# Kernel optimization log

Hardware: AMD Instinct MI355X
Metric: run time of the kernel (lower is better)

Reference implementation:

```python
import jax, jax.numpy as jnp
import numpy as np

B, L, D, H = 2, 2048, 512, 8
Dh = D // H


def setup_inputs() -> dict:
    key = jax.random.key(0)
    ks = jax.random.split(key, 12)
    def lin(i):
        W = jax.random.normal(ks[i], (D, D), dtype=jnp.float32) * (1.0 / np.sqrt(D))
        b = jax.random.normal(ks[i + 1], (D,), dtype=jnp.float32) * 0.02
        return W, b
    Wq, bq = lin(0)
    Wk, bk = lin(2)
    Wv, bv = lin(4)
    Wo, bo = lin(6)
    wave_real = jax.random.normal(ks[8], (B, L, D), dtype=jnp.float32)
    wave_imag = jax.random.normal(ks[9], (B, L, D), dtype=jnp.float32)
    return {"wave_real": wave_real, "wave_imag": wave_imag,
            "Wq": Wq, "bq": bq, "Wk": Wk, "bk": bk,
            "Wv": Wv, "bv": bv, "Wo": Wo, "bo": bo}


def _heads(x):
    # (B,L,D) -> (B,H,L,Dh)
    return x.reshape(B, L, H, Dh).transpose(0, 2, 1, 3)


def reference(wave_real, wave_imag, Wq, bq, Wk, bk, Wv, bv, Wo, bo):
    Qr = _heads(wave_real @ Wq.T + bq)
    Qi = _heads(wave_imag @ Wq.T + bq)
    Kr = _heads(wave_real @ Wk.T + bk)
    Ki = _heads(wave_imag @ Wk.T + bk)
    Vr = _heads(wave_real @ Wv.T + bv)
    Vi = _heads(wave_imag @ Wv.T + bv)

    inner_real = jnp.einsum('bhid,bhjd->bhij', Qr, Kr) + jnp.einsum('bhid,bhjd->bhij', Qi, Ki)
    inner_imag = jnp.einsum('bhid,bhjd->bhij', Qr, Ki) - jnp.einsum('bhid,bhjd->bhij', Qi, Kr)

    scores = (inner_real ** 2 + inner_imag ** 2) / np.sqrt(Dh).astype(np.float32)
    attention = jax.nn.softmax(scores, axis=-1)

    phase = jnp.arctan2(inner_imag, inner_real)
    ac = attention * jnp.cos(phase)  # (B,H,L,L)
    as_ = attention * jnp.sin(phase)

    # sum_j att_ij*(Vr_j*cos_ij - Vi_j*sin_ij) -- fused contraction, same math as
    # the original's materialized (B,H,L,L,Dh) rotate-then-sum.
    out_real = jnp.einsum('bhij,bhjd->bhid', ac, Vr) - jnp.einsum('bhij,bhjd->bhid', as_, Vi)
    out_imag = jnp.einsum('bhij,bhjd->bhid', as_, Vr) + jnp.einsum('bhij,bhjd->bhid', ac, Vi)

    out_real = out_real.transpose(0, 2, 1, 3).reshape(B, L, D)
    out_imag = out_imag.transpose(0, 2, 1, 3).reshape(B, L, D)
    return (out_real @ Wo.T + bo, out_imag @ Wo.T + bo, attention)
```

## Files before the change

kernel.cpp:

```cpp
#include <hip/hip_runtime.h>

typedef unsigned short u16;
typedef unsigned int   u32;
typedef __attribute__((ext_vector_type(4)))  u16   us4;
typedef __attribute__((ext_vector_type(8)))  u16   us8;
typedef __attribute__((ext_vector_type(8)))  short s8v;
typedef __attribute__((ext_vector_type(16))) float f32x16;

#define L_   2048
#define D_   512
#define H_   8
#define PE_  2097152ull

#define MATE    2097152ull
#define BHE     131072u
#define VT_OFF  33554432ull
#define ORH_OFF 41943040ull
#define ORL_OFF 46137344ull
#define OIH_OFF 50331648ull
#define OIL_OFF 54525952ull
#define LV_OFF  58720256ull

#define XRH_O 16777216ull
#define XRL_O 20971520ull
#define XIH_O 25165824ull
#define XIL_O 29360128ull

#define MFMA32(a,b,c) __builtin_amdgcn_mfma_f32_32x32x16_bf16(a,b,c,0,0,0)
#define ROWOF(r,hi) (((r)&3) + 8*((r)>>2) + 4*(hi))

__device__ __forceinline__ u16 f2bf(float x){
    u32 u = __float_as_uint(x);
    u += 0x7FFFu + ((u>>16)&1u);
    return (u16)(u>>16);
}
__device__ __forceinline__ float bf2f(u16 h){ return __uint_as_float(((u32)h)<<16); }

__device__ __forceinline__ void glds16(const void* gsrc, void* ldst)
{
    __builtin_amdgcn_global_load_lds(
        (const __attribute__((address_space(1))) u32*)(unsigned long long)gsrc,
        (__attribute__((address_space(3))) u32*)(u32)(unsigned long long)ldst,
        16, 0, 0);
}
__device__ __forceinline__ void glds_mat(unsigned char* Lp, u32 matOff,
                                         const u16* g, int rowBase, int lane)
{
    const char* gb = (const char*)(g + (size_t)rowBase * 64);
    #pragma unroll
    for (int s = 0; s < 8; ++s)
        glds16(gb + s*1024 + lane*16, Lp + matOff + s*1024);
}
__device__ __forceinline__ void glds_vt(unsigned char* Lp, u32 matOff,
                                        const u16* g, int j0, int lane, int s0)
{
    #pragma unroll
    for (int s = 0; s < 4; ++s) {
        int seg = s0 + s;
        int dh  = seg*8 + (lane >> 3);
        const char* gp = (const char*)g + (size_t)dh*4096 + (size_t)j0*2 + (lane & 7)*16;
        glds16(gp, Lp + matOff + seg*1024u);
    }
}

__global__ __launch_bounds__(256)
void split_prep_kernel(const float* __restrict__ wr, const float* __restrict__ wi,
                       unsigned char* __restrict__ outb)
{
    const int z = blockIdx.y;
    const float* src = z ? wi : wr;
    u16* hg = (u16*)(outb + (z ? XIH_O : XRH_O));
    u16* lg = (u16*)(outb + (z ? XIL_O : XRL_O));
    const size_t idx4 = ((size_t)blockIdx.x * 256 + threadIdx.x) * 4;
    float4 v = *(const float4*)&src[idx4];
    float vv[4] = { v.x, v.y, v.z, v.w };
    us4 h, l;
    #pragma unroll
    for (int c = 0; c < 4; ++c) {
        u16 hb = f2bf(vv[c]);
        h[c] = hb;
        l[c] = f2bf(vv[c] - bf2f(hb));
    }
    *(us4*)&hg[idx4] = h;
    *(us4*)&lg[idx4] = l;
}

__device__ __forceinline__ s8v ldfrag(const unsigned char* Lp, u32 matOff, u32 row, u32 colb)
{
    return *(const s8v*)(Lp + matOff + row*128u + (colb ^ ((row&7u)<<4)));
}

__global__ __launch_bounds__(256, 2)
void proj_mfma_kernel(const unsigned char* __restrict__ scr,
                      const float* __restrict__ Wq, const float* __restrict__ Wk,
                      const float* __restrict__ Wv,
                      const float* __restrict__ bq, const float* __restrict__ bk,
                      const float* __restrict__ bv,
                      u16* __restrict__ qk, u16* __restrict__ vt)
{
    const int z = blockIdx.z;
    const u16* Ah_g = (const u16*)(scr + ((z & 1) ? XIH_O : XRH_O));
    const u16* Al_g = (const u16*)(scr + ((z & 1) ? XIL_O : XRL_O));
    const int wsel = z >> 1;
    const float* Wf; const float* bias;
    if (wsel == 0)      { Wf = Wq; bias = bq; }
    else if (wsel == 1) { Wf = Wk; bias = bk; }
    else                { Wf = Wv; bias = bv; }
    const bool four = (wsel < 2);

    const int m0 = blockIdx.x * 128;
    const int n0 = blockIdx.y * 64;

    __shared__ __align__(16) unsigned char L[49152];
    enum : u32 { AH=0, AL=16384, BH=32768, BL=40960 };

    const int tid  = threadIdx.x;
    const int lane = tid & 63;
    const int wid  = tid >> 6;
    const int wr   = wid >> 1, wc = wid & 1;
    const int l31  = lane & 31;
    const int hi   = lane >> 5;
    const u32 rowA0 = (u32)(wr*64 + l31);
    const u32 rowB  = (u32)(wc*32 + l31);

    f32x16 c0, c1;
    #pragma unroll
    for (int r = 0; r < 16; ++r) { c0[r] = 0.f; c1[r] = 0.f; }

    const int ch = tid & 7, r0 = tid >> 3;

    for (int k0 = 0; k0 < 512; k0 += 64) {
        __syncthreads();
        #pragma unroll
        for (int rr = 0; rr < 4; ++rr) {
            u32 row = (u32)(rr*32 + r0);
            u32 dst = row*128u + (((u32)ch<<4) ^ ((row&7u)<<4));
            us8 vh = *(const us8*)(Ah_g + (size_t)(m0 + row)*512 + k0 + ch*8);
            *(us8*)(L + AH + dst) = vh;
            if (four) {
                us8 vl = *(const us8*)(Al_g + (size_t)(m0 + row)*512 + k0 + ch*8);
                *(us8*)(L + AL + dst) = vl;
            }
        }
        #pragma unroll
        for (int rr = 0; rr < 2; ++rr) {
            u32 row = (u32)(rr*32 + r0);
            const float* src = Wf + (size_t)(n0 + row)*512 + k0 + ch*8;
            float4 v0 = *(const float4*)src;
            float4 v1 = *(const float4*)(src + 4);
            float vv[8] = { v0.x,v0.y,v0.z,v0.w, v1.x,v1.y,v1.z,v1.w };
            us8 hv, lv;
            #pragma unroll
            for (int j = 0; j < 8; ++j) {
                u16 hb = f2bf(vv[j]);
                hv[j] = hb;
                lv[j] = f2bf(vv[j] - bf2f(hb));
            }
            u32 dst = row*128u + (((u32)ch<<4) ^ ((row&7u)<<4));
            *(us8*)(L + BH + dst) = hv;
            if (four) *(us8*)(L + BL + dst) = lv;
        }
        __syncthreads();

        #pragma unroll
        for (int ks = 0; ks < 4; ++ks) {
            u32 colb = (u32)(ks*32 + hi*16);
            s8v a0h = ldfrag(L, AH, rowA0,      colb);
            s8v a1h = ldfrag(L, AH, rowA0 + 32, colb);
            s8v bh_ = ldfrag(L, BH, rowB,       colb);
            c0 = MFMA32(a0h, bh_, c0);
            c1 = MFMA32(a1h, bh_, c1);
            if (four) {
                s8v a0l = ldfrag(L, AL, rowA0,      colb);
                s8v a1l = ldfrag(L, AL, rowA0 + 32, colb);
                s8v bl_ = ldfrag(L, BL, rowB,       colb);
                c0 = MFMA32(a0h, bl_, c0); c0 = MFMA32(a0l, bh_, c0); c0 = MFMA32(a0l, bl_, c0);
                c1 = MFMA32(a1h, bl_, c1); c1 = MFMA32(a1l, bh_, c1); c1 = MFMA32(a1l, bl_, c1);
            }
        }
    }

    const int n  = n0 + wc*32 + l31;
    const float bvv = bias[n];
    const int h  = n >> 6, dh = n & 63;

    if (z < 4) {
        u16* hg = qk + (size_t)(2*z)   * MATE;
        u16* lg = qk + (size_t)(2*z+1) * MATE;
        #pragma unroll
        for (int f = 0; f < 2; ++f) {
            const f32x16& c = f ? c1 : c0;
            #pragma unroll
            for (int r = 0; r < 16; ++r) {
                int m  = m0 + wr*64 + 32*f + ROWOF(r, hi);
                int b_ = m >> 11, i = m & 2047;
                size_t idx = (size_t)(b_*8 + h)*BHE + (size_t)i*64 + (dh ^ ((i&7)<<3));
                float v = c[r] + bvv;
                u16 hb = f2bf(v);
                hg[idx] = hb;
                lg[idx] = f2bf(v - bf2f(hb));
            }
        }
    } else {
        u16* vg = vt + (size_t)(z & 1) * MATE;
        #pragma unroll
        for (int f = 0; f < 2; ++f) {
            const f32x16& c = f ? c1 : c0;
            #pragma unroll
            for (int g = 0; g < 4; ++g) {
                int mb = m0 + wr*64 + 32*f + 8*g + 4*hi;
                int b_ = mb >> 11, ib = mb & 2047;
                us4 pv;
                #pragma unroll
                for (int j = 0; j < 4; ++j) pv[j] = f2bf(c[4*g + j] + bvv);
                int ibs = ib ^ ((dh & 7) << 3);
                *(us4*)&vg[(size_t)(b_*8 + h)*BHE + (size_t)dh*2048 + ibs] = pv;
            }
        }
    }
}

__global__ __launch_bounds__(256, 2)
void attn_mfma_kernel(const u16* __restrict__ qk,
                      const u16* __restrict__ vt,
                      float* __restrict__ attnbuf,
                      u16* __restrict__ orh, u16* __restrict__ orl,
                      u16* __restrict__ oih, u16* __restrict__ oil,
                      float* __restrict__ l_out)
{
    const int bh = blockIdx.x;
    const int i0 = blockIdx.y * 64;
    const int tid  = threadIdx.x;
    const int lane = tid & 63;
    const int wid  = tid >> 6;
    const int wr   = wid >> 1, wc = wid & 1;
    const int l31  = lane & 31;
    const int hi   = lane >> 5;
    const u32 rowA = wr*32 + l31;
    const u32 rowB = wc*32 + l31;

    __shared__ __align__(16) unsigned char L[49152];
    enum : u32 { QRH=0, QIH=8192,
                 KRH=16384, KRL=24576, KIH=32768, KIL=40960,
                 VRo=16384, VIo=24576,
                 PAC=32768, PAS=40960 };
    float* sc = (float*)(L + PAC);

    const u16* qrh = qk + 0*MATE + (size_t)bh*BHE;
    const u16* qrl = qk + 1*MATE + (size_t)bh*BHE;
    const u16* qih = qk + 2*MATE + (size_t)bh*BHE;
    const u16* qil = qk + 3*MATE + (size_t)bh*BHE;
    const u16* krh = qk + 4*MATE + (size_t)bh*BHE;
    const u16* krl = qk + 5*MATE + (size_t)bh*BHE;
    const u16* kih = qk + 6*MATE + (size_t)bh*BHE;
    const u16* kil = qk + 7*MATE + (size_t)bh*BHE;
    const u16* vtr = vt + 0*MATE + (size_t)bh*BHE;
    const u16* vti = vt + 1*MATE + (size_t)bh*BHE;

    {
        const u16* qsrc = (wid == 0) ? qrh : (wid == 1) ? qih : (wid == 2) ? qrl : qil;
        const u32  qdst = (wid == 0) ? QRH : (wid == 1) ? QIH : (wid == 2) ? KRH : KRL;
        glds_mat(L, qdst, qsrc, i0, lane);
    }
    __syncthreads();
    s8v qfl[2][4];
    #pragma unroll
    for (int ks = 0; ks < 4; ++ks) {
        u32 colb = (u32)(ks*32 + hi*16);
        qfl[0][ks] = ldfrag(L, KRH, rowA, colb);
        qfl[1][ks] = ldfrag(L, KRL, rowA, colb);
    }

    float mxv[16];
    #pragma unroll
    for (int r = 0; r < 16; ++r) mxv[r] = 0.f;

    const u16* s1src = (wid & 1) ? kih : krh;
    const u32  s1off = 16384u + (u32)wid * 8192u;

    for (int jp = 0; jp < 16; ++jp) {
        __syncthreads();
        glds_mat(L, s1off, s1src, (2*jp + (wid >> 1))*64, lane);
        __syncthreads();
        __builtin_amdgcn_s_setprio(1);
        #pragma unroll
        for (int half = 0; half < 2; ++half) {
            const u32 kR = half ? KIH : KRH;
            const u32 kI = half ? KIL : KRL;
            f32x16 ir, ip, in_;
            #pragma unroll
            for (int r = 0; r < 16; ++r) { ir[r]=0.f; ip[r]=0.f; in_[r]=0.f; }
            #pragma unroll
            for (int ks = 0; ks < 4; ++ks) {
                u32 colb = ks*32 + hi*16;
                s8v aR = ldfrag(L, QRH, rowA, colb);
                s8v aI = ldfrag(L, QIH, rowA, colb);
                s8v bR = ldfrag(L, kR,  rowB, colb);
                s8v bI = ldfrag(L, kI,  rowB, colb);
                ir  = MFMA32(aR, bR, ir);
                ir  = MFMA32(aI, bI, ir);
                ip  = MFMA32(aR, bI, ip);
                in_ = MFMA32(aI, bR, in_);
            }
            #pragma unroll
            for (int r = 0; r < 16; ++r) {
                float xr = ir[r], xi = ip[r] - in_[r];
                float q = xr*xr + xi*xi;
                mxv[r] = fmaxf(mxv[r], q * 0.125f);
            }
        }
        __builtin_amdgcn_s_setprio(0);
    }
    #pragma unroll
    for (int m = 1; m < 32; m <<= 1)
        #pragma unroll
        for (int r = 0; r < 16; ++r) mxv[r] = fmaxf(mxv[r], __shfl_xor(mxv[r], m));

    __syncthreads();
    #pragma unroll
    for (int r = 0; r < 16; ++r)
        if (l31 == r) sc[wc*64 + wr*32 + ROWOF(r,hi)] = mxv[r];
    __syncthreads();
    float mfin[16];
    #pragma unroll
    for (int r = 0; r < 16; ++r) {
        u32 row = wr*32 + ROWOF(r,hi);
        mfin[r] = fmaxf(sc[row], sc[64 + row]);
    }

    f32x16 ore, oim;
    float lp[16];
    #pragma unroll
    for (int r = 0; r < 16; ++r) { ore[r]=0.f; oim[r]=0.f; lp[r]=0.f; }

    const u16* s2src = (wid == 0) ? krh : (wid == 1) ? krl : (wid == 2) ? kih : kil;
    const u32  s2off = 16384u + (u32)wid * 8192u;
    const u16* vsrc  = (wid < 2) ? vtr : vti;
    const u32  voff  = (wid < 2) ? VRo : VIo;
    const int  vseg  = (wid & 1) * 4;

    u16* ebase = (u16*)(attnbuf + (size_t)bh*4194304ull + (size_t)i0*2048);

    for (int jt = 0; jt < 32; ++jt) {
        const int j0 = jt * 64;
        __syncthreads();
        glds_mat(L, s2off, s2src, j0, lane);
        __syncthreads();

        f32x16 ir, ip, in_;
        #pragma unroll
        for (int r = 0; r < 16; ++r) { ir[r]=0.f; ip[r]=0.f; in_[r]=0.f; }
        __builtin_amdgcn_s_setprio(1);
        #pragma unroll
        for (int ks = 0; ks < 4; ++ks) {
            u32 colb = ks*32 + hi*16;
            s8v aRH = ldfrag(L, QRH, rowA, colb);
            s8v aIH = ldfrag(L, QIH, rowA, colb);
            s8v aRL = qfl[0][ks];
            s8v aIL = qfl[1][ks];
            s8v bRH = ldfrag(L, KRH, rowB, colb);
            s8v bRL = ldfrag(L, KRL, rowB, colb);
            s8v bIH = ldfrag(L, KIH, rowB, colb);
            s8v bIL = ldfrag(L, KIL, rowB, colb);
            ir = MFMA32(aRH, bRH, ir); ir = MFMA32(aRH, bRL, ir); ir = MFMA32(aRL, bRH, ir);
            ir = MFMA32(aIH, bIH, ir); ir = MFMA32(aIH, bIL, ir); ir = MFMA32(aIL, bIH, ir);
            ip  = MFMA32(aRH, bIH, ip);  ip  = MFMA32(aRH, bIL, ip);  ip  = MFMA32(aRL, bIH, ip);
            in_ = MFMA32(aIH, bRH, in_); in_ = MFMA32(aIH, bRL, in_); in_ = MFMA32(aIL, bRH, in_);
        }
        __builtin_amdgcn_s_setprio(0);
        __syncthreads();

        glds_vt(L, voff, vsrc, j0, lane, vseg);

        #pragma unroll
        for (int r = 0; r < 16; ++r) {
            float xr = ir[r], xi = ip[r] - in_[r];
            float q  = fmaf(xr, xr, xi*xi);
            float e  = __expf(fmaf(q, 0.125f, -mfin[r]));
            lp[r] += e;
            float iv = rsqrtf(q);
            float t  = e * iv;
            float pc = (q > 0.f) ? xr*t : e;
            float ps = (q > 0.f) ? xi*t : 0.0f;
            u32 rowloc = wr*32 + ROWOF(r,hi);
            ebase[(size_t)rowloc*4096 + j0 + wc*32 + l31] = f2bf(e);
            u32 colb2 = (wc*32 + l31)*2;
            *(u16*)(L + PAC + rowloc*128u + (colb2 ^ ((rowloc&7u)<<4))) = f2bf(pc);
            *(u16*)(L + PAS + rowloc*128u + (colb2 ^ ((rowloc&7u)<<4))) = f2bf(ps);
        }
        __syncthreads();

        __builtin_amdgcn_s_setprio(1);
        #pragma unroll
        for (int ks = 0; ks < 4; ++ks) {
            u32 colb = ks*32 + hi*16;
            s8v aC = ldfrag(L, PAC, rowA, colb);
            s8v aS = ldfrag(L, PAS, rowA, colb);
            s8v vR = ldfrag(L, VRo, rowB, colb);
            s8v vI = ldfrag(L, VIo, rowB, colb);
            s8v vN = vI ^ (short)0x8000;
            ore = MFMA32(aC, vR, ore); ore = MFMA32(aS, vN, ore);
            oim = MFMA32(aS, vR, oim); oim = MFMA32(aC, vI, oim);
        }
        __builtin_amdgcn_s_setprio(0);
    }

    #pragma unroll
    for (int m = 1; m < 32; m <<= 1)
        #pragma unroll
        for (int r = 0; r < 16; ++r) lp[r] += __shfl_xor(lp[r], m);

    __syncthreads();
    #pragma unroll
    for (int r = 0; r < 16; ++r)
        if (l31 == r) sc[wc*64 + wr*32 + ROWOF(r,hi)] = lp[r];
    __syncthreads();

    const int b_ = bh >> 3, h = bh & 7;
    const size_t cb = (size_t)h*64 + wc*32 + l31;
    #pragma unroll
    for (int r = 0; r < 16; ++r) {
        u32 row = wr*32 + ROWOF(r,hi);
        float ls = sc[row] + sc[64 + row];
        if (wc == 0 && l31 == 0) l_out[(size_t)bh*2048 + i0 + row] = ls;
        float inv = 1.0f / ls;
        size_t idx = ((size_t)b_*2048 + i0 + row)*512 + cb;
        float vr = ore[r] * inv;
        float vi = oim[r] * inv;
        u16 hr = f2bf(vr); orh[idx] = hr; orl[idx] = f2bf(vr - bf2f(hr));
        u16 hw = f2bf(vi); oih[idx] = hw; oil[idx] = f2bf(vi - bf2f(hw));
    }
}

__global__ __launch_bounds__(256)
void expand_attn_kernel(float* __restrict__ attnbuf, const float* __restrict__ l)
{
    const int row = blockIdx.x;
    const float inv = 1.f / l[row];
    float* rowf = attnbuf + (size_t)row * 2048;
    const us8 ev = *(const us8*)((const u16*)rowf + threadIdx.x * 8);
    __syncthreads();
    float4 o0, o1;
    o0.x = bf2f(ev[0])*inv; o0.y = bf2f(ev[1])*inv;
    o0.z = bf2f(ev[2])*inv; o0.w = bf2f(ev[3])*inv;
    o1.x = bf2f(ev[4])*inv; o1.y = bf2f(ev[5])*inv;
    o1.z = bf2f(ev[6])*inv; o1.w = bf2f(ev[7])*inv;
    float* dst = rowf + threadIdx.x * 8;
    *(float4*)dst       = o0;
    *(float4*)(dst + 4) = o1;
}

__global__ __launch_bounds__(256, 2)
void oproj_mfma_kernel(const unsigned char* __restrict__ wsb,
                       const float* __restrict__ Wo, const float* __restrict__ bo,
                       float* __restrict__ out)
{
    const int z = blockIdx.z;
    const u16* Ah_g = (const u16*)(wsb + (z ? OIH_OFF : ORH_OFF));
    const u16* Al_g = (const u16*)(wsb + (z ? OIL_OFF : ORL_OFF));
    float* outp = out + (size_t)z * PE_;

    const int m0 = blockIdx.x * 128;
    const int n0 = blockIdx.y * 64;

    __shared__ __align__(16) unsigned char L[49152];
    enum : u32 { AH=0, AL=16384, BH=32768, BL=40960 };

    const int tid  = threadIdx.x;
    const int lane = tid & 63;
    const int wid  = tid >> 6;
    const int wr   = wid >> 1, wc = wid & 1;
    const int l31  = lane & 31;
    const int hi   = lane >> 5;
    const u32 rowA0 = (u32)(wr*64 + l31);
    const u32 rowB  = (u32)(wc*32 + l31);

    f32x16 c0, c1;
    #pragma unroll
    for (int r = 0; r < 16; ++r) { c0[r] = 0.f; c1[r] = 0.f; }

    const int ch = tid & 7, r0 = tid >> 3;

    for (int k0 = 0; k0 < 512; k0 += 64) {
        __syncthreads();
        #pragma unroll
        for (int rr = 0; rr < 4; ++rr) {
            u32 row = (u32)(rr*32 + r0);
            u32 dst = row*128u + (((u32)ch<<4) ^ ((row&7u)<<4));
            us8 vh = *(const us8*)(Ah_g + (size_t)(m0 + row)*512 + k0 + ch*8);
            us8 vl = *(const us8*)(Al_g + (size_t)(m0 + row)*512 + k0 + ch*8);
            *(us8*)(L + AH + dst) = vh;
            *(us8*)(L + AL + dst) = vl;
        }
        #pragma unroll
        for (int rr = 0; rr < 2; ++rr) {
            u32 row = (u32)(rr*32 + r0);
            const float* src = Wo + (size_t)(n0 + row)*512 + k0 + ch*8;
            float4 v0 = *(const float4*)src;
            float4 v1 = *(const float4*)(src + 4);
            float vv[8] = { v0.x,v0.y,v0.z,v0.w, v1.x,v1.y,v1.z,v1.w };
            us8 hv, lv;
            #pragma unroll
            for (int j = 0; j < 8; ++j) {
                u16 hb = f2bf(vv[j]);
                hv[j] = hb;
                lv[j] = f2bf(vv[j] - bf2f(hb));
            }
            u32 dst = row*128u + (((u32)ch<<4) ^ ((row&7u)<<4));
            *(us8*)(L + BH + dst) = hv;
            *(us8*)(L + BL + dst) = lv;
        }
        __syncthreads();

        #pragma unroll
        for (int ks = 0; ks < 4; ++ks) {
            u32 colb = (u32)(ks*32 + hi*16);
            s8v a0h = ldfrag(L, AH, rowA0,      colb);
            s8v a1h = ldfrag(L, AH, rowA0 + 32, colb);
            s8v a0l = ldfrag(L, AL, rowA0,      colb);
            s8v a1l = ldfrag(L, AL, rowA0 + 32, colb);
            s8v bh_ = ldfrag(L, BH, rowB,       colb);
            s8v bl_ = ldfrag(L, BL, rowB,       colb);
            c0 = MFMA32(a0h, bh_, c0); c0 = MFMA32(a0h, bl_, c0); c0 = MFMA32(a0l, bh_, c0);
            c1 = MFMA32(a1h, bh_, c1); c1 = MFMA32(a1h, bl_, c1); c1 = MFMA32(a1l, bh_, c1);
        }
    }

    const int n = n0 + wc*32 + l31;
    const float bvv = bo[n];
    #pragma unroll
    for (int f = 0; f < 2; ++f) {
        const f32x16& c = f ? c1 : c0;
        #pragma unroll
        for (int r = 0; r < 16; ++r) {
            int m = m0 + wr*64 + 32*f + ROWOF(r, hi);
            outp[(size_t)m*512 + n] = c[r] + bvv;
        }
    }
}

extern "C" void kernel_launch(void* const* d_in, const int* in_sizes, int n_in,
                              void* d_out, int out_size, void* d_ws, size_t ws_size,
                              hipStream_t stream)
{
    const float* wave_real = (const float*)d_in[0];
    const float* wave_imag = (const float*)d_in[1];
    const float* Wq = (const float*)d_in[2]; const float* bq = (const float*)d_in[3];
    const float* Wk = (const float*)d_in[4]; const float* bk = (const float*)d_in[5];
    const float* Wv = (const float*)d_in[6]; const float* bv = (const float*)d_in[7];
    const float* Wo = (const float*)d_in[8]; const float* bo = (const float*)d_in[9];
    float* out = (float*)d_out;
    unsigned char* outb = (unsigned char*)d_out;
    unsigned char* wsb  = (unsigned char*)d_ws;

    float* attnbuf = out + 2*PE_;

    split_prep_kernel<<<dim3(2048, 2), dim3(256), 0, stream>>>(wave_real, wave_imag, outb);

    proj_mfma_kernel<<<dim3(32, 8, 6), dim3(256), 0, stream>>>(
        outb, Wq, Wk, Wv, bq, bk, bv,
        (u16*)wsb, (u16*)(wsb + VT_OFF));

    attn_mfma_kernel<<<dim3(16, 32), dim3(256), 0, stream>>>(
        (const u16*)wsb, (const u16*)(wsb + VT_OFF), attnbuf,
        (u16*)(wsb + ORH_OFF), (u16*)(wsb + ORL_OFF),
        (u16*)(wsb + OIH_OFF), (u16*)(wsb + OIL_OFF),
        (float*)(wsb + LV_OFF));

    expand_attn_kernel<<<dim3(32768), dim3(256), 0, stream>>>(
        attnbuf, (const float*)(wsb + LV_OFF));

    oproj_mfma_kernel<<<dim3(32, 8, 2), dim3(256), 0, stream>>>(
        wsb, Wo, bo, out);
}
```

Baseline: 336.2 us.

## Process two key tiles per barrier round in attention passes

Grows LDS from 48KB to 80KB so that each sync round loads and processes 128 keys (two 64-key tiles) instead of 64, in both the max pass (four tiles per round instead of two) and the main softmax/PV pass. This halves the number of __syncthreads barriers and global-to-LDS load rounds per block and gives more independent MFMA work between barriers. The cost is higher LDS use and register pressure from holding two score tiles at once, which may reduce occupancy.

```diff
diff --git a/kernel.cpp b/kernel.cpp
--- a/kernel.cpp
+++ b/kernel.cpp
@@ -51,12 +51,11 @@
     for (int s = 0; s < 8; ++s)
         glds16(gb + s*1024 + lane*16, Lp + matOff + s*1024);
 }
-__device__ __forceinline__ void glds_vt(unsigned char* Lp, u32 matOff,
-                                        const u16* g, int j0, int lane, int s0)
-{
-    #pragma unroll
-    for (int s = 0; s < 4; ++s) {
-        int seg = s0 + s;
+__device__ __forceinline__ void glds_vt_full(unsigned char* Lp, u32 matOff,
+                                             const u16* g, int j0, int lane)
+{
+    #pragma unroll
+    for (int seg = 0; seg < 8; ++seg) {
         int dh  = seg*8 + (lane >> 3);
         const char* gp = (const char*)g + (size_t)dh*4096 + (size_t)j0*2 + (lane & 7)*16;
         glds16(gp, Lp + matOff + seg*1024u);
@@ -239,12 +238,9 @@
     const u32 rowA = wr*32 + l31;
     const u32 rowB = wc*32 + l31;
 
-    __shared__ __align__(16) unsigned char L[49152];
-    enum : u32 { QRH=0, QIH=8192,
-                 KRH=16384, KRL=24576, KIH=32768, KIL=40960,
-                 VRo=16384, VIo=24576,
-                 PAC=32768, PAS=40960 };
-    float* sc = (float*)(L + PAC);
+    __shared__ __align__(16) unsigned char L[81920];
+    enum : u32 { QRH=0, QIH=8192, KB=16384 };
+    float* sc = (float*)(L + KB);
 
     const u16* qrh = qk + 0*MATE + (size_t)bh*BHE;
     const u16* qrl = qk + 1*MATE + (size_t)bh*BHE;
@@ -259,7 +255,7 @@
 
     {
         const u16* qsrc = (wid == 0) ? qrh : (wid == 1) ? qih : (wid == 2) ? qrl : qil;
-        const u32  qdst = (wid == 0) ? QRH : (wid == 1) ? QIH : (wid == 2) ? KRH : KRL;
+        const u32  qdst = (wid == 0) ? QRH : (wid == 1) ? QIH : (wid == 2) ? (KB) : (KB + 8192);
         glds_mat(L, qdst, qsrc, i0, lane);
     }
     __syncthreads();
@@ -267,26 +263,24 @@
     #pragma unroll
     for (int ks = 0; ks < 4; ++ks) {
         u32 colb = (u32)(ks*32 + hi*16);
-        qfl[0][ks] = ldfrag(L, KRH, rowA, colb);
-        qfl[1][ks] = ldfrag(L, KRL, rowA, colb);
+        qfl[0][ks] = ldfrag(L, KB,        rowA, colb);
+        qfl[1][ks] = ldfrag(L, KB + 8192, rowA, colb);
     }
 
     float mxv[16];
     #pragma unroll
     for (int r = 0; r < 16; ++r) mxv[r] = 0.f;
 
-    const u16* s1src = (wid & 1) ? kih : krh;
-    const u32  s1off = 16384u + (u32)wid * 8192u;
-
-    for (int jp = 0; jp < 16; ++jp) {
-        __syncthreads();
-        glds_mat(L, s1off, s1src, (2*jp + (wid >> 1))*64, lane);
+    for (int gp = 0; gp < 8; ++gp) {
+        __syncthreads();
+        glds_mat(L, KB + (u32)(2*wid)*8192u,   krh, (4*gp + wid)*64, lane);
+        glds_mat(L, KB + (u32)(2*wid+1)*8192u, kih, (4*gp + wid)*64, lane);
         __syncthreads();
         __builtin_amdgcn_s_setprio(1);
         #pragma unroll
-        for (int half = 0; half < 2; ++half) {
-            const u32 kR = half ? KIH : KRH;
-            const u32 kI = half ? KIL : KRL;
+        for (int t = 0; t < 4; ++t) {
+            const u32 kR = KB + (u32)(2*t)*8192u;
+            const u32 kI = kR + 8192u;
             f32x16 ir, ip, in_;
             #pragma unroll
             for (int r = 0; r < 16; ++r) { ir[r]=0.f; ip[r]=0.f; in_[r]=0.f; }
@@ -334,47 +328,73 @@
     for (int r = 0; r < 16; ++r) { ore[r]=0.f; oim[r]=0.f; lp[r]=0.f; }
 
     const u16* s2src = (wid == 0) ? krh : (wid == 1) ? krl : (wid == 2) ? kih : kil;
-    const u32  s2off = 16384u + (u32)wid * 8192u;
-    const u16* vsrc  = (wid < 2) ? vtr : vti;
-    const u32  voff  = (wid < 2) ? VRo : VIo;
-    const int  vseg  = (wid & 1) * 4;
+    const u16* vsrc2 = (wid & 1) ? vti : vtr;
 
     u16* ebase = (u16*)(attnbuf + (size_t)bh*4194304ull + (size_t)i0*2048);
 
-    for (int jt = 0; jt < 32; ++jt) {
-        const int j0 = jt * 64;
-        __syncthreads();
-        glds_mat(L, s2off, s2src, j0, lane);
-        __syncthreads();
-
-        f32x16 ir, ip, in_;
-        #pragma unroll
-        for (int r = 0; r < 16; ++r) { ir[r]=0.f; ip[r]=0.f; in_[r]=0.f; }
+    for (int pt = 0; pt < 16; ++pt) {
+        const int j0a = pt*128, j0b = j0a + 64;
+        __syncthreads();
+        glds_mat(L, KB + (u32)wid*8192u,          s2src, j0a, lane);
+        glds_mat(L, KB + 32768u + (u32)wid*8192u, s2src, j0b, lane);
+        __syncthreads();
+
+        f32x16 xra, xia, xrb, xib;
         __builtin_amdgcn_s_setprio(1);
-        #pragma unroll
-        for (int ks = 0; ks < 4; ++ks) {
-            u32 colb = ks*32 + hi*16;
-            s8v aRH = ldfrag(L, QRH, rowA, colb);
-            s8v aIH = ldfrag(L, QIH, rowA, colb);
-            s8v aRL = qfl[0][ks];
-            s8v aIL = qfl[1][ks];
-            s8v bRH = ldfrag(L, KRH, rowB, colb);
-            s8v bRL = ldfrag(L, KRL, rowB, colb);
-            s8v bIH = ldfrag(L, KIH, rowB, colb);
-            s8v bIL = ldfrag(L, KIL, rowB, colb);
-            ir = MFMA32(aRH, bRH, ir); ir = MFMA32(aRH, bRL, ir); ir = MFMA32(aRL, bRH, ir);
-            ir = MFMA32(aIH, bIH, ir); ir = MFMA32(aIH, bIL, ir); ir = MFMA32(aIL, bIH, ir);
-            ip  = MFMA32(aRH, bIH, ip);  ip  = MFMA32(aRH, bIL, ip);  ip  = MFMA32(aRL, bIH, ip);
-            in_ = MFMA32(aIH, bRH, in_); in_ = MFMA32(aIH, bRL, in_); in_ = MFMA32(aIL, bRH, in_);
+        {
+            f32x16 ir, ip, in_;
+            #pragma unroll
+            for (int r = 0; r < 16; ++r) { ir[r]=0.f; ip[r]=0.f; in_[r]=0.f; }
+            #pragma unroll
+            for (int ks = 0; ks < 4; ++ks) {
+                u32 colb = ks*32 + hi*16;
+                s8v aRH = ldfrag(L, QRH, rowA, colb);
+                s8v aIH = ldfrag(L, QIH, rowA, colb);
+                s8v aRL = qfl[0][ks];
+                s8v aIL = qfl[1][ks];
+                s8v bRH = ldfrag(L, KB + 0,     rowB, colb);
+                s8v bRL = ldfrag(L, KB + 8192,  rowB, colb);
+                s8v bIH = ldfrag(L, KB + 16384, rowB, colb);
+                s8v bIL = ldfrag(L, KB + 24576, rowB, colb);
+                ir = MFMA32(aRH, bRH, ir); ir = MFMA32(aRH, bRL, ir); ir = MFMA32(aRL, bRH, ir);
+                ir = MFMA32(aIH, bIH, ir); ir = MFMA32(aIH, bIL, ir); ir = MFMA32(aIL, bIH, ir);
+                ip  = MFMA32(aRH, bIH, ip);  ip  = MFMA32(aRH, bIL, ip);  ip  = MFMA32(aRL, bIH, ip);
+                in_ = MFMA32(aIH, bRH, in_); in_ = MFMA32(aIH, bRL, in_); in_ = MFMA32(aIL, bRH, in_);
+            }
+            #pragma unroll
+            for (int r = 0; r < 16; ++r) { xra[r] = ir[r]; xia[r] = ip[r] - in_[r]; }
+        }
+        {
+            f32x16 ir, ip, in_;
+            #pragma unroll
+            for (int r = 0; r < 16; ++r) { ir[r]=0.f; ip[r]=0.f; in_[r]=0.f; }
+            #pragma unroll
+            for (int ks = 0; ks < 4; ++ks) {
+                u32 colb = ks*32 + hi*16;
+                s8v aRH = ldfrag(L, QRH, rowA, colb);
+                s8v aIH = ldfrag(L, QIH, rowA, colb);
+                s8v aRL = qfl[0][ks];
+                s8v aIL = qfl[1][ks];
+                s8v bRH = ldfrag(L, KB + 32768,         rowB, colb);
+                s8v bRL = ldfrag(L, KB + 32768 + 8192,  rowB, colb);
+                s8v bIH = ldfrag(L, KB + 32768 + 16384, rowB, colb);
+                s8v bIL = ldfrag(L, KB + 32768 + 24576, rowB, colb);
+                ir = MFMA32(aRH, bRH, ir); ir = MFMA32(aRH, bRL, ir); ir = MFMA32(aRL, bRH, ir);
+                ir = MFMA32(aIH, bIH, ir); ir = MFMA32(aIH, bIL, ir); ir = MFMA32(aIL, bIH, ir);
+                ip  = MFMA32(aRH, bIH, ip);  ip  = MFMA32(aRH, bIL, ip);  ip  = MFMA32(aRL, bIH, ip);
+                in_ = MFMA32(aIH, bRH, in_); in_ = MFMA32(aIH, bRL, in_); in_ = MFMA32(aIL, bRH, in_);
+            }
+            #pragma unroll
+            for (int r = 0; r < 16; ++r) { xrb[r] = ir[r]; xib[r] = ip[r] - in_[r]; }
         }
         __builtin_amdgcn_s_setprio(0);
         __syncthreads();
 
-        glds_vt(L, voff, vsrc, j0, lane, vseg);
+        glds_vt_full(L, KB + (u32)wid*8192u, vsrc2, (wid < 2) ? j0a : j0b, lane);
 
         #pragma unroll
         for (int r = 0; r < 16; ++r) {
-            float xr = ir[r], xi = ip[r] - in_[r];
+            float xr = xra[r], xi = xia[r];
             float q  = fmaf(xr, xr, xi*xi);
             float e  = __expf(fmaf(q, 0.125f, -mfin[r]));
             lp[r] += e;
@@ -383,10 +403,26 @@
             float pc = (q > 0.f) ? xr*t : e;
             float ps = (q > 0.f) ? xi*t : 0.0f;
             u32 rowloc = wr*32 + ROWOF(r,hi);
-            ebase[(size_t)rowloc*4096 + j0 + wc*32 + l31] = f2bf(e);
+            ebase[(size_t)rowloc*4096 + j0a + wc*32 + l31] = f2bf(e);
             u32 colb2 = (wc*32 + l31)*2;
-            *(u16*)(L + PAC + rowloc*128u + (colb2 ^ ((rowloc&7u)<<4))) = f2bf(pc);
-            *(u16*)(L + PAS + rowloc*128u + (colb2 ^ ((rowloc&7u)<<4))) = f2bf(ps);
+            *(u16*)(L + KB + 32768u + rowloc*128u + (colb2 ^ ((rowloc&7u)<<4))) = f2bf(pc);
+            *(u16*)(L + KB + 40960u + rowloc*128u + (colb2 ^ ((rowloc&7u)<<4))) = f2bf(ps);
+        }
+        #pragma unroll
+        for (int r = 0; r < 16; ++r) {
+            float xr = xrb[r], xi = xib[r];
+            float q  = fmaf(xr, xr, xi*xi);
+            float e  = __expf(fmaf(q, 0.125f, -mfin[r]));
+            lp[r] += e;
+            float iv = rsqrtf(q);
+            float t  = e * iv;
+            float pc = (q > 0.f) ? xr*t : e;
+            float ps = (q > 0.f) ? xi*t : 0.0f;
+            u32 rowloc = wr*32 + ROWOF(r,hi);
+            ebase[(size_t)rowloc*4096 + j0b + wc*32 + l31] = f2bf(e);
+            u32 colb2 = (wc*32 + l31)*2;
+            *(u16*)(L + KB + 49152u + rowloc*128u + (colb2 ^ ((rowloc&7u)<<4))) = f2bf(pc);
+            *(u16*)(L + KB + 57344u + rowloc*128u + (colb2 ^ ((rowloc&7u)<<4))) = f2bf(ps);
         }
         __syncthreads();
 
@@ -394,10 +430,21 @@
         #pragma unroll
         for (int ks = 0; ks < 4; ++ks) {
             u32 colb = ks*32 + hi*16;
-            s8v aC = ldfrag(L, PAC, rowA, colb);
-            s8v aS = ldfrag(L, PAS, rowA, colb);
-            s8v vR = ldfrag(L, VRo, rowB, colb);
-            s8v vI = ldfrag(L, VIo, rowB, colb);
+            s8v aC = ldfrag(L, KB + 32768u, rowA, colb);
+            s8v aS = ldfrag(L, KB + 40960u, rowA, colb);
+            s8v vR = ldfrag(L, KB + 0,      rowB, colb);
+            s8v vI = ldfrag(L, KB + 8192u,  rowB, colb);
+            s8v vN = vI ^ (short)0x8000;
+            ore = MFMA32(aC, vR, ore); ore = MFMA32(aS, vN, ore);
+            oim = MFMA32(aS, vR, oim); oim = MFMA32(aC, vI, oim);
+        }
+        #pragma unroll
+        for (int ks = 0; ks < 4; ++ks) {
+            u32 colb = ks*32 + hi*16;
+            s8v aC = ldfrag(L, KB + 49152u, rowA, colb);
+            s8v aS = ldfrag(L, KB + 57344u, rowA, colb);
+            s8v vR = ldfrag(L, KB + 16384u, rowB, colb);
+            s8v vI = ldfrag(L, KB + 24576u, rowB, colb);
             s8v vN = vI ^ (short)0x8000;
             ore = MFMA32(aC, vR, ore); ore = MFMA32(aS, vN, ore);
             oim = MFMA32(aS, vR, oim); oim = MFMA32(aC, vI, oim);
```

Result: slower. 637.5 us (+89.6%).

## Double-buffer K tiles in max pass and prefetch next K tile in main loop

Applied to the files above, without the earlier changes.

Grows shared memory from 48KB to 80KB so the max-finding pass can ping-pong between two K buffers, issuing the next tile's global-to-LDS load before computing on the current one. In the main loop, the next K tile load is issued alongside the V load after the score MFMAs, and V and P get their own LDS regions. This removes a barrier pair per iteration and overlaps load latency with compute. The larger LDS footprint may lower occupancy per CU.

```diff
diff --git a/kernel.cpp b/kernel.cpp
--- a/kernel.cpp
+++ b/kernel.cpp
@@ -239,11 +239,12 @@
     const u32 rowA = wr*32 + l31;
     const u32 rowB = wc*32 + l31;
 
-    __shared__ __align__(16) unsigned char L[49152];
+    __shared__ __align__(16) unsigned char L[81920];
     enum : u32 { QRH=0, QIH=8192,
-                 KRH=16384, KRL=24576, KIH=32768, KIL=40960,
-                 VRo=16384, VIo=24576,
-                 PAC=32768, PAS=40960 };
+                 KR0=16384,
+                 S1A=16384, S1B=49152,
+                 VRo=49152, VIo=57344,
+                 PAC=65536, PAS=73728 };
     float* sc = (float*)(L + PAC);
 
     const u16* qrh = qk + 0*MATE + (size_t)bh*BHE;
@@ -259,7 +260,7 @@
 
     {
         const u16* qsrc = (wid == 0) ? qrh : (wid == 1) ? qih : (wid == 2) ? qrl : qil;
-        const u32  qdst = (wid == 0) ? QRH : (wid == 1) ? QIH : (wid == 2) ? KRH : KRL;
+        const u32  qdst = (wid == 0) ? QRH : (wid == 1) ? QIH : (wid == 2) ? KR0 : (KR0 + 8192);
         glds_mat(L, qdst, qsrc, i0, lane);
     }
     __syncthreads();
@@ -267,26 +268,31 @@
     #pragma unroll
     for (int ks = 0; ks < 4; ++ks) {
         u32 colb = (u32)(ks*32 + hi*16);
-        qfl[0][ks] = ldfrag(L, KRH, rowA, colb);
-        qfl[1][ks] = ldfrag(L, KRL, rowA, colb);
-    }
+        qfl[0][ks] = ldfrag(L, KR0,        rowA, colb);
+        qfl[1][ks] = ldfrag(L, KR0 + 8192, rowA, colb);
+    }
+    __syncthreads();
+
+    const u16* s1src = (wid & 1) ? kih : krh;
+
+    glds_mat(L, S1A + (u32)wid*8192u, s1src, (0 + (wid >> 1))*64, lane);
 
     float mxv[16];
     #pragma unroll
     for (int r = 0; r < 16; ++r) mxv[r] = 0.f;
 
-    const u16* s1src = (wid & 1) ? kih : krh;
-    const u32  s1off = 16384u + (u32)wid * 8192u;
-
-    for (int jp = 0; jp < 16; ++jp) {
-        __syncthreads();
-        glds_mat(L, s1off, s1src, (2*jp + (wid >> 1))*64, lane);
-        __syncthreads();
+    for (int g = 0; g < 16; ++g) {
+        const u32 base = (g & 1) ? S1B : S1A;
+        __syncthreads();
+        if (g < 15) {
+            const u32 nbase = (g & 1) ? S1A : S1B;
+            glds_mat(L, nbase + (u32)wid*8192u, s1src, (2*(g+1) + (wid >> 1))*64, lane);
+        }
         __builtin_amdgcn_s_setprio(1);
         #pragma unroll
-        for (int half = 0; half < 2; ++half) {
-            const u32 kR = half ? KIH : KRH;
-            const u32 kI = half ? KIL : KRL;
+        for (int t = 0; t < 2; ++t) {
+            const u32 kR = base + (u32)t*16384u;
+            const u32 kI = kR + 8192u;
             f32x16 ir, ip, in_;
             #pragma unroll
             for (int r = 0; r < 16; ++r) { ir[r]=0.f; ip[r]=0.f; in_[r]=0.f; }
@@ -327,25 +333,25 @@
         u32 row = wr*32 + ROWOF(r,hi);
         mfin[r] = fmaxf(sc[row], sc[64 + row]);
     }
-
-    f32x16 ore, oim;
-    float lp[16];
-    #pragma unroll
-    for (int r = 0; r < 16; ++r) { ore[r]=0.f; oim[r]=0.f; lp[r]=0.f; }
+    __syncthreads();
 
     const u16* s2src = (wid == 0) ? krh : (wid == 1) ? krl : (wid == 2) ? kih : kil;
-    const u32  s2off = 16384u + (u32)wid * 8192u;
     const u16* vsrc  = (wid < 2) ? vtr : vti;
     const u32  voff  = (wid < 2) ? VRo : VIo;
     const int  vseg  = (wid & 1) * 4;
 
+    glds_mat(L, KR0 + (u32)wid*8192u, s2src, 0, lane);
+    __syncthreads();
+
+    f32x16 ore, oim;
+    float lp[16];
+    #pragma unroll
+    for (int r = 0; r < 16; ++r) { ore[r]=0.f; oim[r]=0.f; lp[r]=0.f; }
+
     u16* ebase = (u16*)(attnbuf + (size_t)bh*4194304ull + (size_t)i0*2048);
 
     for (int jt = 0; jt < 32; ++jt) {
         const int j0 = jt * 64;
-        __syncthreads();
-        glds_mat(L, s2off, s2src, j0, lane);
-        __syncthreads();
 
         f32x16 ir, ip, in_;
         #pragma unroll
@@ -358,10 +364,10 @@
             s8v aIH = ldfrag(L, QIH, rowA, colb);
             s8v aRL = qfl[0][ks];
             s8v aIL = qfl[1][ks];
-            s8v bRH = ldfrag(L, KRH, rowB, colb);
-            s8v bRL = ldfrag(L, KRL, rowB, colb);
-            s8v bIH = ldfrag(L, KIH, rowB, colb);
-            s8v bIL = ldfrag(L, KIL, rowB, colb);
+            s8v bRH = ldfrag(L, KR0 + 0,     rowB, colb);
+            s8v bRL = ldfrag(L, KR0 + 8192,  rowB, colb);
+            s8v bIH = ldfrag(L, KR0 + 16384, rowB, colb);
+            s8v bIL = ldfrag(L, KR0 + 24576, rowB, colb);
             ir = MFMA32(aRH, bRH, ir); ir = MFMA32(aRH, bRL, ir); ir = MFMA32(aRL, bRH, ir);
             ir = MFMA32(aIH, bIH, ir); ir = MFMA32(aIH, bIL, ir); ir = MFMA32(aIL, bIH, ir);
             ip  = MFMA32(aRH, bIH, ip);  ip  = MFMA32(aRH, bIL, ip);  ip  = MFMA32(aRL, bIH, ip);
@@ -370,6 +376,7 @@
         __builtin_amdgcn_s_setprio(0);
         __syncthreads();
 
+        if (jt < 31) glds_mat(L, KR0 + (u32)wid*8192u, s2src, j0 + 64, lane);
         glds_vt(L, voff, vsrc, j0, lane, vseg);
 
         #pragma unroll
```

Result: slower. 361.1 us (+7.4%).
